# Kernel optimization log

Hardware: AMD Instinct MI355X
Metric: run time of the kernel (lower is better)

## Reference

```python
import jax, jax.numpy as jnp
import numpy as np

V, E, H, K, B, T = 21128, 256, 256, 21, 64, 512


def setup_inputs() -> dict:
    key = jax.random.key(0)
    ks = jax.random.split(key, 16)
    s = 0.08
    x = jax.random.randint(ks[0], (B, T), 0, V, dtype=jnp.int32)
    y = jax.random.randint(ks[1], (B, T), 0, K, dtype=jnp.int32)
    masks = jnp.ones((B, T), dtype=bool)  # torchcrf requires mask[:,0]=1
    return {
        "x": x, "y": y, "masks": masks,
        "emb": jax.random.normal(ks[2], (V, E), jnp.float32) * s,
        # PyTorch LSTM gate order: i, f, g, o. b = b_ih + b_hh folded.
        "wih_f": jax.random.normal(ks[3], (4 * H, E), jnp.float32) * s,
        "whh_f": jax.random.normal(ks[4], (4 * H, H), jnp.float32) * s,
        "b_f": jax.random.normal(ks[5], (4 * H,), jnp.float32) * s,
        "wih_b": jax.random.normal(ks[6], (4 * H, E), jnp.float32) * s,
        "whh_b": jax.random.normal(ks[7], (4 * H, H), jnp.float32) * s,
        "b_b": jax.random.normal(ks[8], (4 * H,), jnp.float32) * s,
        "wc": jax.random.normal(ks[9], (K, 2 * H), jnp.float32) * s,
        "bc": jax.random.normal(ks[10], (K,), jnp.float32) * s,
        "start": jax.random.normal(ks[11], (K,), jnp.float32) * s,
        "end": jax.random.normal(ks[12], (K,), jnp.float32) * s,
        "trans": jax.random.normal(ks[13], (K, K), jnp.float32) * s,
    }


def _lstm_dir(xe, wih, whh, b):
    # xe: [B,T,E] -> h: [B,T,H]
    pre = jnp.einsum('bte,ge->btg', xe, wih) + b  # [B,T,4H]
    h0 = jnp.zeros((xe.shape[0], whh.shape[1]), xe.dtype)

    def step(carry, p):
        h, c = carry
        g = p + h @ whh.T
        i, f, gg, o = jnp.split(g, 4, axis=-1)
        c = jax.nn.sigmoid(f) * c + jax.nn.sigmoid(i) * jnp.tanh(gg)
        h = jax.nn.sigmoid(o) * jnp.tanh(c)
        return (h, c), h

    _, hs = jax.lax.scan(step, (h0, h0), jnp.swapaxes(pre, 0, 1))
    return jnp.swapaxes(hs, 0, 1)


def _viterbi(em, mask, start, end, trans):
    # em: [B,T,K] -> best tags [B,T]
    b = em.shape[0]
    emT = jnp.swapaxes(em, 0, 1)          # [T,B,K]
    maskT = jnp.swapaxes(mask, 0, 1)      # [T,B]
    score0 = start + emT[0]               # [B,K]

    def step(score, inp):
        e, m = inp
        nxt = score[:, :, None] + trans[None] + e[:, None, :]  # [B,K,K]
        bp = jnp.argmax(nxt, axis=1)
        ns = jnp.max(nxt, axis=1)
        return jnp.where(m[:, None], ns, score), bp

    score, hist = jax.lax.scan(step, score0, (emT[1:], maskT[1:]))
    score = score + end
    last = jnp.argmax(score, axis=1)      # [B]
    bar = jnp.arange(b)

    def back(tag, inp):
        bp, m = inp
        tag = jnp.where(m, bp[bar, tag], tag)
        return tag, tag

    _, tags_rev = jax.lax.scan(back, last, (hist[::-1], maskT[1:][::-1]))
    tags = jnp.concatenate([tags_rev[::-1], last[None]], axis=0)  # [T,B]
    return jnp.swapaxes(tags, 0, 1)


def _crf_llh_mean(em, y, mask, start, end, trans):
    maskf = mask.astype(em.dtype)
    # numerator: score of the gold path
    emt = jnp.take_along_axis(em, y[..., None], axis=-1)[..., 0]   # [B,T]
    tr = trans[y[:, :-1], y[:, 1:]]                                 # [B,T-1]
    num = start[y[:, 0]] + emt[:, 0] + jnp.sum(maskf[:, 1:] * (tr + emt[:, 1:]), axis=1)
    last_idx = jnp.sum(mask.astype(jnp.int32), axis=1) - 1
    last_tag = jnp.take_along_axis(y, last_idx[:, None], axis=1)[:, 0]
    num = num + end[last_tag]
    # denominator: forward algorithm (log partition)
    emT = jnp.swapaxes(em, 0, 1)
    maskT = jnp.swapaxes(mask, 0, 1)
    a0 = start + emT[0]

    def step(a, inp):
        e, m = inp
        nxt = jax.nn.logsumexp(a[:, :, None] + trans[None] + e[:, None, :], axis=1)
        return jnp.where(m[:, None], nxt, a), None

    a, _ = jax.lax.scan(step, a0, (emT[1:], maskT[1:]))
    z = jax.nn.logsumexp(a + end, axis=1)
    return jnp.mean(num - z)  # torchcrf reduction='mean' over batch


def reference(x, y, masks, emb, wih_f, whh_f, b_f, wih_b, whh_b, b_b, wc, bc, start, end, trans):
    xe = emb[x]                                            # [B,T,E]
    hf = _lstm_dir(xe, wih_f, whh_f, b_f)
    hb = _lstm_dir(xe[:, ::-1], wih_b, whh_b, b_b)[:, ::-1]
    h = jnp.concatenate([hf, hb], axis=-1)                 # [B,T,2H]
    em = jnp.einsum('bth,kh->btk', h, wc) + bc             # [B,T,K]
    y_pred = _viterbi(em, masks, start, end, trans)
    loss = _crf_llh_mean(em, y, masks, start, end, trans)
    return (y_pred, loss)
```

## Files before the change

kernel.cpp:

```cpp
#include <hip/hip_runtime.h>

#define T_ 512
#define B_ 64
#define E_ 256
#define H_ 256
#define K_ 21

typedef short          s16x8 __attribute__((ext_vector_type(8)));
typedef unsigned short u16x4 __attribute__((ext_vector_type(4)));
typedef float          f32x4 __attribute__((ext_vector_type(4)));
typedef unsigned long long u64x2 __attribute__((ext_vector_type(2)));

__device__ __attribute__((aligned(16))) unsigned short g_hs[T_ * B_ * 2 * H_];
__device__ __attribute__((aligned(16))) unsigned short g_hbuf[2 * 4 * B_ * H_];
__device__ __attribute__((aligned(16))) float    g_em[T_ * B_ * K_];
__device__ __attribute__((aligned(16))) unsigned short g_wpk[2048 * 256];
__device__ __attribute__((aligned(16))) unsigned short g_hpk[2048 * 256];
__device__ __attribute__((aligned(16))) float g_pre[(size_t)T_ * 128 * 4 * 64 * 4];
__device__ int   g_marker;
__device__ int   g_done_pre;
__device__ int   g_done_lstm;
__device__ int   g_done_dec;
__device__ int   g_timeout;
__device__ float g_sum;

#define CLASS_MASK 0x4000400040004000ULL

__device__ __forceinline__ f32x4 mfma16(s16x8 a, s16x8 b, f32x4 c) {
  return __builtin_amdgcn_mfma_f32_16x16x32_bf16(a, b, c, 0, 0, 0);
}

__device__ __forceinline__ unsigned short f2b(float f) {
  unsigned u = __float_as_uint(f);
  u = (u + 0x7fffu + ((u >> 16) & 1u)) >> 16;
  return (unsigned short)u;
}

__device__ __forceinline__ s16x8 cvt8(const float* p) {
  s16x8 v;
#pragma unroll
  for (int j = 0; j < 8; ++j) v[j] = (short)f2b(p[j]);
  return v;
}

__device__ __forceinline__ s16x8 frag2(unsigned long long a, unsigned long long b) {
  u64x2 t; t[0] = a; t[1] = b;
  return __builtin_bit_cast(s16x8, t);
}

__device__ __forceinline__ const f32x4* pre_tile(int t, int dir, int s, int wn, int wm,
                                                 int lane, int ni, int mi) {
  size_t idx = ((((size_t)t * 128 + dir * 64 + (2 * wn + ni) * 16 + s) * 4)
                + (wm * 2 + mi)) * 64 + lane;
  return (const f32x4*)(g_pre + idx * 4);
}

__global__ void k_zero() {
  int i = blockIdx.x * 256 + threadIdx.x;
  ((unsigned long long*)g_hbuf)[i] = CLASS_MASK;
  if (i == 0) {
    g_marker = 1;
    g_done_pre = 0;
    g_done_lstm = 0;
    g_done_dec = 0;
    g_timeout = 0;
    g_sum = 0.f;
  }
}

__global__ __launch_bounds__(256) void k_prep(
    const float* __restrict__ wih_f, const float* __restrict__ wih_b,
    const float* __restrict__ whh_f, const float* __restrict__ whh_b) {
  const int r = blockIdx.x;
  const int c = threadIdx.x;
  const int rr = r & 1023;
  const float* wi = (r < 1024) ? wih_f : wih_b;
  const float* wh = (r < 1024) ? whh_f : whh_b;
  g_wpk[(size_t)r * 256 + c] = f2b(wi[(size_t)rr * E_ + c]);
  g_hpk[(size_t)r * 256 + c] = f2b(wh[(size_t)rr * H_ + c]);
}

__global__ __launch_bounds__(256) void k_pre(const int* __restrict__ x,
                                             const float* __restrict__ emb) {
  const int t = blockIdx.x;
  const int tid = threadIdx.x;
  const int lane = tid & 63;
  const int wv = tid >> 6;
  const int wm = wv & 1;
  const int wn = wv >> 1;
  const int l15 = lane & 15;
  const int l4 = lane >> 4;
  const int b0 = wm * 32 + l15;
  const int b1 = b0 + 16;

  s16x8 a0[8], a1[8];
  {
    const float* e0 = emb + (size_t)x[b0 * T_ + t] * E_;
    const float* e1 = emb + (size_t)x[b1 * T_ + t] * E_;
#pragma unroll
    for (int kc = 0; kc < 8; ++kc) {
      a0[kc] = cvt8(e0 + kc * 32 + l4 * 8);
      a1[kc] = cvt8(e1 + kc * 32 + l4 * 8);
    }
  }

  for (int ntl = 0; ntl < 64; ++ntl) {
    const int nt = wn * 64 + ntl;
    s16x8 bf[8];
#pragma unroll
    for (int kc = 0; kc < 8; ++kc)
      bf[kc] = *(const s16x8*)(g_wpk + (size_t)(nt * 16 + l15) * 256 + kc * 32 + l4 * 8);
    f32x4 c0 = {0, 0, 0, 0}, c1 = {0, 0, 0, 0};
#pragma unroll
    for (int kc = 0; kc < 8; ++kc) {
      c0 = mfma16(a0[kc], bf[kc], c0);
      c1 = mfma16(a1[kc], bf[kc], c1);
    }
    *(f32x4*)(g_pre + ((((size_t)t * 128 + nt) * 4 + wm * 2 + 0) * 64 + lane) * 4) = c0;
    *(f32x4*)(g_pre + ((((size_t)t * 128 + nt) * 4 + wm * 2 + 1) * 64 + lane) * 4) = c1;
  }
  if (tid == 0) atomicAdd(&g_done_pre, 1);
}

__device__ __forceinline__ void lstm_step(
    int step, int dir, int s, int wv, int lane, int wm, int wn,
    int l15, int l4, int em_m, int em_jg,
    unsigned short* hb4,
    const s16x8 (&bfr)[2][8], const float (&bq)[4][4], float (&cst)[4],
    float* G, f32x4 (&preC)[4], f32x4 (&preN)[4])
{
  const int t = dir ? (T_ - 1 - step) : step;
  const int wbuf = step & 3;
  const int am0 = wm * 32 + l15;
  const int am1 = am0 + 16;
  const unsigned long long M = CLASS_MASK;

  unsigned long long r0[16], r1[16];
  if (step == 0) {
#pragma unroll
    for (int i = 0; i < 16; ++i) { r0[i] = 0ull; r1[i] = 0ull; }
  } else {
    const int rbuf = (step - 1) & 3;
    const unsigned long long want = (((step - 1) >> 2) & 1) ? M : 0ull;
    const unsigned long long* hq = (const unsigned long long*)(hb4 + rbuf * (B_ * H_));
    const unsigned long long* h0q = hq + am0 * (H_ / 4) + l4 * 2;
    const unsigned long long* h1q = hq + am1 * (H_ / 4) + l4 * 2;
    int it = 0;
    for (;;) {
      unsigned long long bad = 0ull;
#pragma unroll
      for (int kc = 0; kc < 8; ++kc) {
        r0[2*kc]   = __hip_atomic_load(h0q + kc*8,   __ATOMIC_RELAXED, __HIP_MEMORY_SCOPE_AGENT);
        r0[2*kc+1] = __hip_atomic_load(h0q + kc*8+1, __ATOMIC_RELAXED, __HIP_MEMORY_SCOPE_AGENT);
        r1[2*kc]   = __hip_atomic_load(h1q + kc*8,   __ATOMIC_RELAXED, __HIP_MEMORY_SCOPE_AGENT);
        r1[2*kc+1] = __hip_atomic_load(h1q + kc*8+1, __ATOMIC_RELAXED, __HIP_MEMORY_SCOPE_AGENT);
      }
#pragma unroll
      for (int kc = 0; kc < 8; ++kc) {
        bad |= (r0[2*kc]   & M) ^ want;
        bad |= (r0[2*kc+1] & M) ^ want;
        bad |= (r1[2*kc]   & M) ^ want;
        bad |= (r1[2*kc+1] & M) ^ want;
      }
      if (__all(bad == 0ull)) break;
      __builtin_amdgcn_s_sleep(1);
      if (++it > (1 << 13)) { if (lane == 0) atomicAdd(&g_timeout, 1); break; }
    }
    if (want) {
#pragma unroll
      for (int i = 0; i < 16; ++i) { r0[i] ^= M; r1[i] ^= M; }
    }
  }

  if (step + 1 < T_) {
    const int tn = dir ? (T_ - 2 - step) : (step + 1);
    preN[0] = *pre_tile(tn, dir, s, wn, wm, lane, 0, 0);
    preN[1] = *pre_tile(tn, dir, s, wn, wm, lane, 1, 0);
    preN[2] = *pre_tile(tn, dir, s, wn, wm, lane, 0, 1);
    preN[3] = *pre_tile(tn, dir, s, wn, wm, lane, 1, 1);
  }

  f32x4 acc00 = preC[0], acc01 = preC[1], acc10 = preC[2], acc11 = preC[3];
#pragma unroll
  for (int kc = 0; kc < 8; ++kc) {
    s16x8 a0 = frag2(r0[2 * kc], r0[2 * kc + 1]);
    s16x8 a1 = frag2(r1[2 * kc], r1[2 * kc + 1]);
    acc00 = mfma16(a0, bfr[0][kc], acc00);
    acc01 = mfma16(a0, bfr[1][kc], acc01);
    acc10 = mfma16(a1, bfr[0][kc], acc10);
    acc11 = mfma16(a1, bfr[1][kc], acc11);
  }

#pragma unroll
  for (int mi = 0; mi < 2; ++mi)
#pragma unroll
    for (int ni = 0; ni < 2; ++ni) {
      f32x4 a = (mi == 0) ? (ni == 0 ? acc00 : acc01) : (ni == 0 ? acc10 : acc11);
#pragma unroll
      for (int r = 0; r < 4; ++r) {
        int m = wm * 32 + mi * 16 + l4 * 4 + r;
        int n = (2 * wn + ni) * 16 + l15;
        G[m * 65 + n] = a[r];
      }
    }
  __syncthreads();

  unsigned short* hrow = hb4 + wbuf * (B_ * H_) + em_m * H_ + s * 16 + em_jg * 4;
  unsigned short* hsro = g_hs + ((size_t)t * B_ + em_m) * (2 * H_) + dir * H_ + s * 16 + em_jg * 4;
  u16x4 hv;
#pragma unroll
  for (int p = 0; p < 4; ++p) {
    int j = em_jg * 4 + p;
    float gi = G[em_m * 65 +  0 + j] + bq[0][p];
    float gf = G[em_m * 65 + 16 + j] + bq[1][p];
    float gg = G[em_m * 65 + 32 + j] + bq[2][p];
    float go = G[em_m * 65 + 48 + j] + bq[3][p];
    float ii = 1.f / (1.f + __expf(-gi));
    float ff = 1.f / (1.f + __expf(-gf));
    float gt = 1.f - 2.f / (__expf(2.f * gg) + 1.f);
    float oo = 1.f / (1.f + __expf(-go));
    float c = ff * cst[p] + ii * gt;
    cst[p] = c;
    float h = oo * (1.f - 2.f / (__expf(2.f * c) + 1.f));
    hv[p] = f2b(h);
  }
  unsigned long long ev = __builtin_bit_cast(unsigned long long, hv);
  if ((step >> 2) & 1) ev ^= M;
  __hip_atomic_store((unsigned long long*)hrow, ev,
                     __ATOMIC_RELAXED, __HIP_MEMORY_SCOPE_AGENT);

  *(u16x4*)hsro = hv;
}

__global__ __launch_bounds__(256, 1) void k_lstm(
    const float* __restrict__ b_f, const float* __restrict__ b_b)
{
  const int wg  = blockIdx.x;
  const int dir = wg & 1;
  const int s   = wg >> 1;
  const int tid = threadIdx.x;
  const int lane = tid & 63;
  const int wv  = tid >> 6;
  const int wm  = wv & 1;
  const int wn  = wv >> 1;
  const int l15 = lane & 15;
  const int l4  = lane >> 4;

  const float* bias = dir ? b_b : b_f;
  unsigned short* hb4 = g_hbuf + (size_t)dir * (4 * B_ * H_);

  s16x8 bfr[2][8];
#pragma unroll
  for (int ni = 0; ni < 2; ++ni) {
    const int nt = dir * 64 + (2 * wn + ni) * 16 + s;
    const unsigned short* wr = g_hpk + (size_t)(nt * 16 + l15) * 256;
#pragma unroll
    for (int kc = 0; kc < 8; ++kc)
      bfr[ni][kc] = *(const s16x8*)(wr + kc * 32 + l4 * 8);
  }

  const int em_m  = tid >> 2;
  const int em_jg = tid & 3;
  float bq[4][4];
#pragma unroll
  for (int q = 0; q < 4; ++q)
#pragma unroll
    for (int p = 0; p < 4; ++p) bq[q][p] = bias[q * H_ + s * 16 + em_jg * 4 + p];
  float cst[4] = {0.f, 0.f, 0.f, 0.f};

  __shared__ float Ga[64 * 65];
  __shared__ float Gb[64 * 65];

  f32x4 preA[4], preB[4];
  {
    const int t0 = dir ? (T_ - 1) : 0;
    preA[0] = *pre_tile(t0, dir, s, wn, wm, lane, 0, 0);
    preA[1] = *pre_tile(t0, dir, s, wn, wm, lane, 1, 0);
    preA[2] = *pre_tile(t0, dir, s, wn, wm, lane, 0, 1);
    preA[3] = *pre_tile(t0, dir, s, wn, wm, lane, 1, 1);
  }

  for (int sp = 0; sp < T_; sp += 2) {
    lstm_step(sp,     dir, s, wv, lane, wm, wn, l15, l4, em_m, em_jg,
              hb4, bfr, bq, cst, Ga, preA, preB);
    lstm_step(sp + 1, dir, s, wv, lane, wm, wn, l15, l4, em_m, em_jg,
              hb4, bfr, bq, cst, Gb, preB, preA);
  }

  __syncthreads();
  if (tid == 0) atomicAdd(&g_done_lstm, 1);
}

__global__ __launch_bounds__(256) void k_em(const float* __restrict__ wc,
                                            const float* __restrict__ bc) {
  const int tid = threadIdx.x;
  const int lane = tid & 63;
  const int wv = tid >> 6;
  const int l15 = lane & 15;
  const int l4 = lane >> 4;
  const int row0 = blockIdx.x * 64 + wv * 16;

  s16x8 bfr[2][16];
#pragma unroll
  for (int ni = 0; ni < 2; ++ni) {
    int n = ni * 16 + l15;
#pragma unroll
    for (int kc = 0; kc < 16; ++kc) {
      s16x8 v;
      if (n < K_) {
        v = cvt8(wc + (size_t)n * (2 * H_) + kc * 32 + l4 * 8);
      } else {
#pragma unroll
        for (int jj = 0; jj < 8; ++jj) v[jj] = 0;
      }
      bfr[ni][kc] = v;
    }
  }

  f32x4 acc0 = {0,0,0,0}, acc1 = {0,0,0,0};
  const unsigned short* arow = g_hs + (size_t)(row0 + l15) * (2 * H_) + l4 * 8;
#pragma unroll
  for (int kc = 0; kc < 16; ++kc) {
    s16x8 a = *(const s16x8*)(arow + kc * 32);
    acc0 = mfma16(a, bfr[0][kc], acc0);
    acc1 = mfma16(a, bfr[1][kc], acc1);
  }
#pragma unroll
  for (int r = 0; r < 4; ++r) {
    int m = l4 * 4 + r;
    g_em[(size_t)(row0 + m) * K_ + l15] = acc0[r] + bc[l15];
    int n1 = 16 + l15;
    if (n1 < K_) g_em[(size_t)(row0 + m) * K_ + n1] = acc1[r] + bc[n1];
  }
}

__global__ void k_decode(const int* __restrict__ y,
                         const float* __restrict__ start, const float* __restrict__ endw,
                         const float* __restrict__ trans,
                         float* __restrict__ out_tags) {
  const int id = blockIdx.x;
  const int k = threadIdx.x;
  const float* em = g_em;
  __shared__ float tr[K_ * K_];
  __shared__ float sc[K_];
  __shared__ unsigned char bp[T_][K_];
  __shared__ short tags[T_];
  __shared__ float zsh;

  for (int i = k; i < K_ * K_; i += 64) tr[i] = trans[i];
  __syncthreads();

  if (id < B_) {
    const int b = id;
    float score = 0.f;
    if (k < K_) score = start[k] + em[(size_t)b * K_ + k];
    __syncthreads();
    for (int t = 1; t < T_; ++t) {
      if (k < K_) sc[k] = score;
      __syncthreads();
      if (k < K_) {
        float e = em[(size_t)(t * B_ + b) * K_ + k];
        float best = -1e30f; int bi = 0;
        for (int k1 = 0; k1 < K_; ++k1) {
          float v = sc[k1] + tr[k1 * K_ + k];
          if (v > best) { best = v; bi = k1; }
        }
        score = best + e;
        bp[t][k] = (unsigned char)bi;
      }
      __syncthreads();
    }
    if (k < K_) sc[k] = score + endw[k];
    __syncthreads();
    if (k == 0) {
      float best = -1e30f; int bi = 0;
      for (int k1 = 0; k1 < K_; ++k1) if (sc[k1] > best) { best = sc[k1]; bi = k1; }
      short tag = (short)bi;
      tags[T_ - 1] = tag;
      for (int t = T_ - 1; t > 0; --t) { tag = (short)bp[t][tag]; tags[t - 1] = tag; }
    }
    __syncthreads();
    for (int t = k; t < T_; t += 64) out_tags[(size_t)b * T_ + t] = (float)tags[t];
    __syncthreads();
    if (k == 0) atomicAdd(&g_done_dec, 1);
  } else {
    const int b = id - B_;
    float al = 0.f;
    if (k < K_) al = start[k] + em[(size_t)b * K_ + k];
    __syncthreads();
    for (int t = 1; t < T_; ++t) {
      if (k < K_) sc[k] = al;
      __syncthreads();
      if (k < K_) {
        float e = em[(size_t)(t * B_ + b) * K_ + k];
        float m = -1e30f;
        for (int k1 = 0; k1 < K_; ++k1) m = fmaxf(m, sc[k1] + tr[k1 * K_ + k]);
        float ssum = 0.f;
        for (int k1 = 0; k1 < K_; ++k1) ssum += __expf(sc[k1] + tr[k1 * K_ + k] - m);
        al = m + __logf(ssum) + e;
      }
      __syncthreads();
    }
    if (k < K_) sc[k] = al + endw[k];
    __syncthreads();
    if (k == 0) {
      float m = -1e30f;
      for (int k1 = 0; k1 < K_; ++k1) m = fmaxf(m, sc[k1]);
      float ssum = 0.f;
      for (int k1 = 0; k1 < K_; ++k1) ssum += __expf(sc[k1] - m);
      zsh = m + __logf(ssum);
    }
    __syncthreads();
    const int* yb = y + b * T_;
    float local = 0.f;
    for (int t = k; t < T_; t += 64) {
      if (t >= 1) {
        int y1 = yb[t], y0 = yb[t - 1];
        local += tr[y0 * K_ + y1] + em[(size_t)(t * B_ + b) * K_ + y1];
      }
    }
    for (int off = 32; off > 0; off >>= 1) local += __shfl_down(local, off, 64);
    if (k == 0) {
      int y0 = yb[0], yl = yb[T_ - 1];
      float num = local + start[y0] + em[(size_t)b * K_ + y0] + endw[yl];
      atomicAdd(&g_sum, (num - zsh) * (1.0f / 64.0f));
      atomicAdd(&g_done_dec, 1);
    }
  }
}

__global__ void k_fin(float* __restrict__ out) {
  float v;
  if (g_marker != 1)             v = -20000.f;
  else if (g_done_pre < 512)     v = -9000.f - (float)g_done_pre;
  else if (g_done_lstm < 32)     v = -3000.f - 32.f * (float)g_done_lstm;
  else if (g_done_dec < 128)     v = -6000.f - 32.f * (float)g_done_dec;
  else if (g_timeout != 0)       v = -2600.f;
  else if (fabsf(g_sum) <= 0.5f) v = -2800.f;
  else                           v = g_sum;
  out[0] = v;
}

extern "C" void kernel_launch(void* const* d_in, const int* in_sizes, int n_in,
                              void* d_out, int out_size, void* d_ws, size_t ws_size,
                              hipStream_t stream) {
  const int*   x     = (const int*)d_in[0];
  const int*   y     = (const int*)d_in[1];
  const float* emb   = (const float*)d_in[3];
  const float* wih_f = (const float*)d_in[4];
  const float* whh_f = (const float*)d_in[5];
  const float* b_f   = (const float*)d_in[6];
  const float* wih_b = (const float*)d_in[7];
  const float* whh_b = (const float*)d_in[8];
  const float* b_b   = (const float*)d_in[9];
  const float* wc    = (const float*)d_in[10];
  const float* bc    = (const float*)d_in[11];
  const float* start = (const float*)d_in[12];
  const float* endw  = (const float*)d_in[13];
  const float* trans = (const float*)d_in[14];

  float* out_f = (float*)d_out;

  k_zero<<<256, 256, 0, stream>>>();
  k_prep<<<2048, 256, 0, stream>>>(wih_f, wih_b, whh_f, whh_b);
  k_pre<<<T_, 256, 0, stream>>>(x, emb);
  k_lstm<<<32, 256, 0, stream>>>(b_f, b_b);
  k_em<<<(T_ * B_) / 64, 256, 0, stream>>>(wc, bc);
  k_decode<<<128, 64, 0, stream>>>(y, start, endw, trans, out_f);
  k_fin<<<1, 1, 0, stream>>>(out_f + (size_t)B_ * T_);
}
```

Baseline: 4.191 ms.

## Issue neighbor h loads before publishing own h slice and bypass global for owned slice

Restructures each LSTM recurrence step so the global loads of the previous hidden state are issued first, and the workgroup's own h slice from the previous step is published afterwards, overlapping the publish with the read latency. The workgroup's own slice is taken from a shared-memory copy instead of waiting for the global round-trip, and the spin check ignores that slice. The __syncthreads calls are replaced with raw s_waitcnt lgkmcnt(0) plus s_barrier asm, with one extra barrier at step end. This adds deferred-store state and a final flush of the last h, and relies on careful ordering of relaxed atomics across workgroups.

```diff
diff --git a/kernel.cpp b/kernel.cpp
--- a/kernel.cpp
+++ b/kernel.cpp
@@ -127,48 +127,46 @@
     int l15, int l4, int em_m, int em_jg,
     unsigned short* hb4,
     const s16x8 (&bfr)[2][8], const float (&bq)[4][4], float (&cst)[4],
-    float* G, f32x4 (&preC)[4], f32x4 (&preN)[4])
+    float* G,
+    unsigned long long* hSprev, unsigned long long* hScur,
+    f32x4 (&preC)[4], f32x4 (&preN)[4],
+    u16x4& hvP, unsigned long long& evP)
 {
-  const int t = dir ? (T_ - 1 - step) : step;
-  const int wbuf = step & 3;
   const int am0 = wm * 32 + l15;
   const int am1 = am0 + 16;
   const unsigned long long M = CLASS_MASK;
+  const int kcO = s >> 1;
+  const bool own = ((l4 >> 1) == (s & 1));
 
   unsigned long long r0[16], r1[16];
+  const unsigned long long* h0q = nullptr;
+  const unsigned long long* h1q = nullptr;
+  unsigned long long want = 0ull;
+
   if (step == 0) {
 #pragma unroll
     for (int i = 0; i < 16; ++i) { r0[i] = 0ull; r1[i] = 0ull; }
   } else {
     const int rbuf = (step - 1) & 3;
-    const unsigned long long want = (((step - 1) >> 2) & 1) ? M : 0ull;
+    want = (((step - 1) >> 2) & 1) ? M : 0ull;
     const unsigned long long* hq = (const unsigned long long*)(hb4 + rbuf * (B_ * H_));
-    const unsigned long long* h0q = hq + am0 * (H_ / 4) + l4 * 2;
-    const unsigned long long* h1q = hq + am1 * (H_ / 4) + l4 * 2;
-    int it = 0;
-    for (;;) {
-      unsigned long long bad = 0ull;
-#pragma unroll
-      for (int kc = 0; kc < 8; ++kc) {
-        r0[2*kc]   = __hip_atomic_load(h0q + kc*8,   __ATOMIC_RELAXED, __HIP_MEMORY_SCOPE_AGENT);
-        r0[2*kc+1] = __hip_atomic_load(h0q + kc*8+1, __ATOMIC_RELAXED, __HIP_MEMORY_SCOPE_AGENT);
-        r1[2*kc]   = __hip_atomic_load(h1q + kc*8,   __ATOMIC_RELAXED, __HIP_MEMORY_SCOPE_AGENT);
-        r1[2*kc+1] = __hip_atomic_load(h1q + kc*8+1, __ATOMIC_RELAXED, __HIP_MEMORY_SCOPE_AGENT);
-      }
-#pragma unroll
-      for (int kc = 0; kc < 8; ++kc) {
-        bad |= (r0[2*kc]   & M) ^ want;
-        bad |= (r0[2*kc+1] & M) ^ want;
-        bad |= (r1[2*kc]   & M) ^ want;
-        bad |= (r1[2*kc+1] & M) ^ want;
-      }
-      if (__all(bad == 0ull)) break;
-      __builtin_amdgcn_s_sleep(1);
-      if (++it > (1 << 13)) { if (lane == 0) atomicAdd(&g_timeout, 1); break; }
-    }
-    if (want) {
-#pragma unroll
-      for (int i = 0; i < 16; ++i) { r0[i] ^= M; r1[i] ^= M; }
+    h0q = hq + am0 * (H_ / 4) + l4 * 2;
+    h1q = hq + am1 * (H_ / 4) + l4 * 2;
+#pragma unroll
+    for (int kc = 0; kc < 8; ++kc) {
+      r0[2*kc]   = __hip_atomic_load(h0q + kc*8,   __ATOMIC_RELAXED, __HIP_MEMORY_SCOPE_AGENT);
+      r0[2*kc+1] = __hip_atomic_load(h0q + kc*8+1, __ATOMIC_RELAXED, __HIP_MEMORY_SCOPE_AGENT);
+      r1[2*kc]   = __hip_atomic_load(h1q + kc*8,   __ATOMIC_RELAXED, __HIP_MEMORY_SCOPE_AGENT);
+      r1[2*kc+1] = __hip_atomic_load(h1q + kc*8+1, __ATOMIC_RELAXED, __HIP_MEMORY_SCOPE_AGENT);
+    }
+    {
+      const int wbP = (step - 1) & 3;
+      unsigned short* hrow = hb4 + wbP * (B_ * H_) + em_m * H_ + s * 16 + em_jg * 4;
+      __hip_atomic_store((unsigned long long*)hrow, evP,
+                         __ATOMIC_RELAXED, __HIP_MEMORY_SCOPE_AGENT);
+      const int tP = dir ? (T_ - step) : (step - 1);
+      unsigned short* hsro = g_hs + ((size_t)tP * B_ + em_m) * (2 * H_) + dir * H_ + s * 16 + em_jg * 4;
+      *(u16x4*)hsro = hvP;
     }
   }
 
@@ -178,6 +176,48 @@
     preN[1] = *pre_tile(tn, dir, s, wn, wm, lane, 1, 0);
     preN[2] = *pre_tile(tn, dir, s, wn, wm, lane, 0, 1);
     preN[3] = *pre_tile(tn, dir, s, wn, wm, lane, 1, 1);
+  }
+
+  if (step > 0) {
+    int it = 0;
+    for (;;) {
+      unsigned long long bad = 0ull;
+#pragma unroll
+      for (int kc = 0; kc < 8; ++kc) {
+        unsigned long long a = r0[2*kc], b = r0[2*kc+1];
+        unsigned long long c = r1[2*kc], d = r1[2*kc+1];
+        if (own && kc == kcO) { a = want; b = want; c = want; d = want; }
+        bad |= (a & M) ^ want;  bad |= (b & M) ^ want;
+        bad |= (c & M) ^ want;  bad |= (d & M) ^ want;
+      }
+      if (__all(bad == 0ull)) break;
+      __builtin_amdgcn_s_sleep(1);
+      if (++it > (1 << 13)) { if (lane == 0) atomicAdd(&g_timeout, 1); break; }
+#pragma unroll
+      for (int kc = 0; kc < 8; ++kc) {
+        r0[2*kc]   = __hip_atomic_load(h0q + kc*8,   __ATOMIC_RELAXED, __HIP_MEMORY_SCOPE_AGENT);
+        r0[2*kc+1] = __hip_atomic_load(h0q + kc*8+1, __ATOMIC_RELAXED, __HIP_MEMORY_SCOPE_AGENT);
+        r1[2*kc]   = __hip_atomic_load(h1q + kc*8,   __ATOMIC_RELAXED, __HIP_MEMORY_SCOPE_AGENT);
+        r1[2*kc+1] = __hip_atomic_load(h1q + kc*8+1, __ATOMIC_RELAXED, __HIP_MEMORY_SCOPE_AGENT);
+      }
+    }
+    if (want) {
+#pragma unroll
+      for (int i = 0; i < 16; ++i) { r0[i] ^= M; r1[i] ^= M; }
+    }
+    {
+      const int pi = (l4 & 1) * 2;
+      unsigned long long sA0 = hSprev[am0 * 4 + pi], sA1 = hSprev[am0 * 4 + pi + 1];
+      unsigned long long sB0 = hSprev[am1 * 4 + pi], sB1 = hSprev[am1 * 4 + pi + 1];
+#pragma unroll
+      for (int kc = 0; kc < 8; ++kc) {
+        bool o = own && (kc == kcO);
+        r0[2*kc]   = o ? sA0 : r0[2*kc];
+        r0[2*kc+1] = o ? sA1 : r0[2*kc+1];
+        r1[2*kc]   = o ? sB0 : r1[2*kc];
+        r1[2*kc+1] = o ? sB1 : r1[2*kc+1];
+      }
+    }
   }
 
   f32x4 acc00 = preC[0], acc01 = preC[1], acc10 = preC[2], acc11 = preC[3];
@@ -203,10 +243,8 @@
         G[m * 65 + n] = a[r];
       }
     }
-  __syncthreads();
-
-  unsigned short* hrow = hb4 + wbuf * (B_ * H_) + em_m * H_ + s * 16 + em_jg * 4;
-  unsigned short* hsro = g_hs + ((size_t)t * B_ + em_m) * (2 * H_) + dir * H_ + s * 16 + em_jg * 4;
+  asm volatile("s_waitcnt lgkmcnt(0)\n\ts_barrier" ::: "memory");
+
   u16x4 hv;
 #pragma unroll
   for (int p = 0; p < 4; ++p) {
@@ -224,12 +262,12 @@
     float h = oo * (1.f - 2.f / (__expf(2.f * c) + 1.f));
     hv[p] = f2b(h);
   }
+  hScur[em_m * 4 + em_jg] = __builtin_bit_cast(unsigned long long, hv);
   unsigned long long ev = __builtin_bit_cast(unsigned long long, hv);
   if ((step >> 2) & 1) ev ^= M;
-  __hip_atomic_store((unsigned long long*)hrow, ev,
-                     __ATOMIC_RELAXED, __HIP_MEMORY_SCOPE_AGENT);
-
-  *(u16x4*)hsro = hv;
+  hvP = hv;
+  evP = ev;
+  asm volatile("s_waitcnt lgkmcnt(0)\n\ts_barrier" ::: "memory");
 }
 
 __global__ __launch_bounds__(256, 1) void k_lstm(
@@ -270,6 +308,8 @@
 
   __shared__ float Ga[64 * 65];
   __shared__ float Gb[64 * 65];
+  __shared__ unsigned long long hSa[64 * 4];
+  __shared__ unsigned long long hSb[64 * 4];
 
   f32x4 preA[4], preB[4];
   {
@@ -280,11 +320,20 @@
     preA[3] = *pre_tile(t0, dir, s, wn, wm, lane, 1, 1);
   }
 
+  u16x4 hvP = {0, 0, 0, 0};
+  unsigned long long evP = 0ull;
+
   for (int sp = 0; sp < T_; sp += 2) {
     lstm_step(sp,     dir, s, wv, lane, wm, wn, l15, l4, em_m, em_jg,
-              hb4, bfr, bq, cst, Ga, preA, preB);
+              hb4, bfr, bq, cst, Ga, hSb, hSa, preA, preB, hvP, evP);
     lstm_step(sp + 1, dir, s, wv, lane, wm, wn, l15, l4, em_m, em_jg,
-              hb4, bfr, bq, cst, Gb, preB, preA);
+              hb4, bfr, bq, cst, Gb, hSa, hSb, preB, preA, hvP, evP);
+  }
+
+  {
+    const int tl = dir ? 0 : (T_ - 1);
+    unsigned short* hsro = g_hs + ((size_t)tl * B_ + em_m) * (2 * H_) + dir * H_ + s * 16 + em_jg * 4;
+    *(u16x4*)hsro = hvP;
   }
 
   __syncthreads();
```

Result: slower. 6.198 ms (+47.9%).
